# Performance work log

Hardware: AMD Instinct MI355X
Metric: run time of the kernel (lower is better)

## Reference

```python
import jax, jax.numpy as jnp
import numpy as np
import math

SR = 16000        # sample_rate
HOP = 512         # hop_length
FMIN = 20.0
N_BINS = 84
BPO = 12          # bins_per_octave
Q = 1.0 / (2.0 ** (1.0 / BPO) - 1.0)


def setup_inputs() -> dict:
    key = jax.random.key(0)
    waveform = jax.random.normal(key, (2560000,), dtype=jnp.float32)
    return {"waveform": waveform}


def _bin_kernel(wl: int, freq: float, dtype):
    """Windowed single-DFT-bin kernel matching torch.stft row `freq_bin`.
    Returns (2,1,wl) conv kernel: [real, imag] parts of conj(e^{-2pi i f n / wl}) * hann.
    """
    n = np.arange(wl)
    # torch.hann_window default is periodic: 0.5*(1 - cos(2*pi*n/N))
    w = 0.5 - 0.5 * np.cos(2.0 * np.pi * n / wl)
    fb = min(int(freq * wl / SR), wl // 2)  # onesided stft has wl//2+1 rows
    ang = 2.0 * np.pi * fb * n / wl
    kr = (w * np.cos(ang)).astype(np.float32)
    ki = (-w * np.sin(ang)).astype(np.float32)
    return jnp.asarray(np.stack([kr, ki])[:, None, :], dtype=dtype)


def reference(waveform) -> jnp.ndarray:
    L = waveform.shape[-1]
    num_frames = (L - HOP) // HOP + 1  # matches torch code's frame count
    rows = []
    for k in range(N_BINS):
        freq = FMIN * 2.0 ** (k / BPO)
        wl = min(int(SR * Q / freq), L // 4)
        if wl < 32:  # torch code skips these bins (row stays zero)
            rows.append(jnp.zeros((num_frames,), waveform.dtype))
            continue
        pad = wl // 2  # torch.stft center=True reflect padding
        xpad = jnp.pad(waveform, (pad, pad), mode="reflect")
        kern = _bin_kernel(wl, freq, waveform.dtype)
        # strided correlation == extracting one DFT bin of every stft frame
        out = jax.lax.conv_general_dilated(
            xpad[None, None, :], kern, window_strides=(HOP,), padding="VALID"
        )[0]  # (2, n_frames_k)
        mag = jnp.sqrt(out[0] ** 2 + out[1] ** 2)
        mf = min(mag.shape[0], num_frames)
        rows.append(jnp.zeros((num_frames,), waveform.dtype).at[:mf].set(mag[:mf]))
    return jnp.stack(rows)[None]  # (1, n_bins, num_frames)
```

## Files before the change

### kernel.cpp

```cpp
#include <hip/hip_runtime.h>
#include <math.h>

#define L_IN   2560000
#define HOP    512
#define NB     84
#define NF     5000
#define PAD0   6726
#define XPLEN  2573452
#define XBLEN2 2637824
#define NTIL   80
#define SLOTS  7
#define NBLK   (NTIL*SLOTS)
#define TSTEPS 251

#define XB_NB  1288
#define AG_NB  502

#define LDS_SZ 70656

#define XB_B 0
#define AG_B 5275648
#define P_B  7331840

typedef short bf16x8 __attribute__((ext_vector_type(8)));
typedef float f32x16 __attribute__((ext_vector_type(16)));

__device__ inline unsigned short f2bf(float f) {
  unsigned int u = __float_as_uint(f);
  return (unsigned short)((u + 0x7fffu + ((u >> 16) & 1u)) >> 16);
}

__device__ inline void load16(void* l, const void* g) {
  __builtin_amdgcn_global_load_lds((const __attribute__((address_space(1))) void*)g,
                                   (__attribute__((address_space(3))) void*)l, 16, 0, 0);
}

__global__ __launch_bounds__(256) void k_prep(const float* __restrict__ x,
                                              unsigned short* __restrict__ xb,
                                              unsigned short* __restrict__ Ag) {
  if (blockIdx.x < XB_NB) {
    int i8 = (blockIdx.x * 256 + threadIdx.x) * 8;
    bf16x8 o;
    int u0 = i8 - PAD0;
    if (u0 >= 0 && u0 + 8 <= L_IN) {
      const float2* p = (const float2*)(x + u0);
#pragma unroll
      for (int j = 0; j < 4; ++j) {
        float2 v = p[j];
        o[2 * j]     = (short)f2bf(v.x);
        o[2 * j + 1] = (short)f2bf(v.y);
      }
    } else {
#pragma unroll
      for (int j = 0; j < 8; ++j) {
        int i = i8 + j;
        float v = 0.f;
        if (i < XPLEN) {
          int u = i - PAD0;
          if (u < 0) u = -u;
          else if (u >= L_IN) u = 2 * L_IN - 2 - u;
          v = x[u];
        }
        o[j] = (short)f2bf(v);
      }
    }
    *(bf16x8*)(xb + i8) = o;
  } else {
    int g = (blockIdx.x - XB_NB) * 256 + threadIdx.x;
    int s = g >> 9, w = g & 511;
    int im = w >> 8, kk = (w >> 6) & 3, lane = w & 63;
    int mt  = (s < 211) ? 0 : ((s < 245) ? 1 : 2);
    int mst = (mt == 0) ? 0 : ((mt == 1) ? 211 : 245);
    int kst = (mt == 0) ? 0 : ((mt == 1) ? 5632 : 6528);
    int tap0 = kst + (s - mst) * 64 + kk * 16 + ((lane >> 5) << 3);
    int row = im * 32 + (lane & 31);
    int bin = mt * 32 + (row >> 1);
    bf16x8 vv;
    if (bin >= NB) {
#pragma unroll
      for (int j = 0; j < 8; ++j) vv[j] = 0;
    } else {
      double q    = 1.0 / (pow(2.0, 1.0 / 12.0) - 1.0);
      double freq = 20.0 * pow(2.0, (double)bin / 12.0);
      int wl = (int)(16000.0 * q / freq);
      if (wl > L_IN / 4) wl = L_IN / 4;
      int pad = wl >> 1;
      int fbq = (int)(freq * (double)wl / 16000.0);
      if (fbq > wl / 2) fbq = wl / 2;
      int isIm = row & 1;
      float invwl = 1.0f / (float)wl;
#pragma unroll
      for (int j = 0; j < 8; ++j) {
        int n = tap0 + j - (PAD0 - pad);
        float v = 0.f;
        if (n >= 0 && n < wl) {
          float wn = 0.5f - 0.5f * cosf(6.2831853071795865f * ((float)n * invwl));
          int m = (fbq * n) % wl;
          float a = 6.2831853071795865f * ((float)m * invwl);
          v = isIm ? (-wn * sinf(a)) : (wn * cosf(a));
        }
        vv[j] = (short)f2bf(v);
      }
    }
    *(bf16x8*)(Ag + ((size_t)s * 4096 + im * 2048 + kk * 512 + lane * 8)) = vv;
  }
}

struct AF { bf16x8 f[2][4]; };

__device__ inline void loadA(AF& a, const char* Ag, int s, int lane) {
  const char* p = Ag + ((size_t)s << 13) + lane * 16;
#pragma unroll
  for (int im = 0; im < 2; ++im)
#pragma unroll
    for (int kk = 0; kk < 4; ++kk)
      a.f[im][kk] = *(const bf16x8*)(p + im * 4096 + kk * 1024);
}

__device__ inline void stepC(const AF& a, int l, int lane, const char* Bw,
                             f32x16 acc[2][2]) {
  bf16x8 bf[2][4];
  int tb = l * 128 + ((lane >> 5) << 4);
#pragma unroll
  for (int in_ = 0; in_ < 2; ++in_) {
    int ob = (in_ * 32 + (lane & 31)) * 1024 + tb;
#pragma unroll
    for (int kk = 0; kk < 4; ++kk) {
      int o = ob + kk * 32;
      o ^= ((o >> 10) & 15) << 4;
      bf[in_][kk] = *(const bf16x8*)(Bw + o);
    }
  }
  __builtin_amdgcn_s_setprio(1);
#pragma unroll
  for (int kk = 0; kk < 4; ++kk)
#pragma unroll
    for (int im = 0; im < 2; ++im)
#pragma unroll
      for (int in_ = 0; in_ < 2; ++in_)
        acc[im][in_] = __builtin_amdgcn_mfma_f32_32x32x16_bf16(
            a.f[im][kk], bf[in_][kk], acc[im][in_], 0, 0, 0);
  __builtin_amdgcn_s_setprio(0);
}

__global__ __launch_bounds__(256, 2) void k_gemm(const unsigned short* __restrict__ Ag,
                                                 const unsigned short* __restrict__ xb,
                                                 float* __restrict__ P,
                                                 float* __restrict__ out) {
  extern __shared__ char lds[];
  const int tid = threadIdx.x, lane = tid & 63, wv = tid >> 6;

  int bid = blockIdx.x;
  int lid = (bid & 7) * (NBLK / 8) + (bid >> 3);
  int nt = lid / SLOTS, c = lid - nt * SLOTS;
  const int gs_[7] = {0, 43, 85, 127, 169, 211, 245};
  const int ns_[7] = {43, 42, 42, 42, 42, 34, 6};
  const int kb_[7] = {0, 2752, 5440, 8128, 10816, 5632, 6528};
  int gs = gs_[c], ns = ns_[c], kb = kb_[c];
  int nch = (64512 + 128 * ns + 1023) >> 10;

  const char* xsrc = (const char*)xb + (size_t)nt * 65536 + (size_t)kb * 2;
  for (int ci = wv; ci < nch; ci += 4)
    load16(lds + ci * 1024, xsrc + ci * 1024 + ((lane * 16) ^ ((ci & 15) << 4)));
  __builtin_amdgcn_sched_barrier(0);

  const char* Ab = (const char*)Ag;
  int nks = (ns - wv + 3) >> 2;
  AF a0, a1, a2;
  int s0 = gs + wv, s1 = gs + wv + 4, s2 = gs + wv + 8;
  loadA(a0, Ab, s0 > 250 ? 250 : s0, lane);
  loadA(a1, Ab, s1 > 250 ? 250 : s1, lane);
  loadA(a2, Ab, s2 > 250 ? 250 : s2, lane);

  f32x16 acc[2][2];
#pragma unroll
  for (int i = 0; i < 2; ++i)
#pragma unroll
    for (int j = 0; j < 2; ++j)
#pragma unroll
      for (int e = 0; e < 16; ++e) acc[i][j][e] = 0.f;

  asm volatile("s_waitcnt vmcnt(24)" ::: "memory");
  __syncthreads();

  int i = 0;
  while (i + 3 <= nks) {
    stepC(a0, wv + 4 * i, lane, lds, acc);
    if (i + 3 < nks) loadA(a0, Ab, gs + wv + 4 * (i + 3), lane);
    stepC(a1, wv + 4 * (i + 1), lane, lds, acc);
    if (i + 4 < nks) loadA(a1, Ab, gs + wv + 4 * (i + 4), lane);
    stepC(a2, wv + 4 * (i + 2), lane, lds, acc);
    if (i + 5 < nks) loadA(a2, Ab, gs + wv + 4 * (i + 5), lane);
    i += 3;
  }
  if (i < nks)     stepC(a0, wv + 4 * i, lane, lds, acc);
  if (i + 1 < nks) stepC(a1, wv + 4 * (i + 1), lane, lds, acc);
  if (i + 2 < nks) stepC(a2, wv + 4 * (i + 2), lane, lds, acc);

  __syncthreads();
  float* Cw = (float*)(lds + wv * 16384);
#pragma unroll
  for (int im = 0; im < 2; ++im)
#pragma unroll
    for (int in_ = 0; in_ < 2; ++in_) {
      f32x16 v = acc[im][in_];
      int col = in_ * 32 + (lane & 31);
      int rb  = im * 32 + ((lane >> 5) << 2);
#pragma unroll
      for (int r = 0; r < 16; ++r) {
        int row = rb + (r & 3) + 8 * (r >> 2);
        Cw[row * 64 + col] = v[r];
      }
    }
  __syncthreads();
  const float* L0 = (const float*)lds;
  if (c < 5) {
    float* Pb = P + ((size_t)(nt * 5 + c) << 12);
#pragma unroll
    for (int e = 0; e < 16; ++e) {
      int idx = e * 256 + tid;
      Pb[idx] = L0[idx] + L0[idx + 4096] + L0[idx + 8192] + L0[idx + 12288];
    }
  } else {
    int bb = (c == 5) ? 32 : 64;
#pragma unroll
    for (int e = 0; e < 8; ++e) {
      int p = e * 256 + tid;
      int bl = p >> 6, fl = p & 63;
      int r0 = (bl * 2) * 64 + fl, r1 = r0 + 64;
      float re = L0[r0] + L0[r0 + 4096] + L0[r0 + 8192] + L0[r0 + 12288];
      float iv = L0[r1] + L0[r1 + 4096] + L0[r1 + 8192] + L0[r1 + 12288];
      int b = bb + bl, col = nt * 64 + fl;
      if (b < NB && col < NF)
        out[(size_t)b * NF + col] = sqrtf(re * re + iv * iv);
    }
  }
}

__global__ __launch_bounds__(256) void k_mag(const float* __restrict__ P,
                                             float* __restrict__ out) {
  int col = blockIdx.x * 256 + threadIdx.x;
  int b = blockIdx.y;
  if (col >= NF) return;
  int nt = col >> 6, fl = col & 63;
  const float* Pt = P + ((size_t)(nt * 5) << 12);
  float re = 0.f, iv = 0.f;
#pragma unroll
  for (int c = 0; c < 5; ++c) {
    const float* Pb = Pt + ((size_t)c << 12);
    re += Pb[(2 * b) * 64 + fl];
    iv += Pb[(2 * b + 1) * 64 + fl];
  }
  out[(size_t)b * NF + col] = sqrtf(re * re + iv * iv);
}

extern "C" void kernel_launch(void* const* d_in, const int* in_sizes, int n_in,
                              void* d_out, int out_size, void* d_ws, size_t ws_size,
                              hipStream_t stream) {
  const float* x = (const float*)d_in[0];
  char* ws = (char*)d_ws;
  unsigned short* xb = (unsigned short*)(ws + XB_B);
  unsigned short* Ag = (unsigned short*)(ws + AG_B);
  float* P           = (float*)(ws + P_B);
  float* out = (float*)d_out;

  hipFuncSetAttribute((const void*)k_gemm,
                      hipFuncAttributeMaxDynamicSharedMemorySize, LDS_SZ);

  hipLaunchKernelGGL(k_prep, dim3(XB_NB + AG_NB), dim3(256), 0, stream, x, xb, Ag);
  hipLaunchKernelGGL(k_gemm, dim3(NBLK), dim3(256), LDS_SZ, stream, Ag, xb, P, out);
  hipLaunchKernelGGL(k_mag, dim3(20, 32), dim3(256), 0, stream, P, out);
}
```

Before: 33.14 us.

## Widen GEMM frame tile to 128 columns with 8-wave blocks

```diff
diff --git a/kernel.cpp b/kernel.cpp
--- a/kernel.cpp
+++ b/kernel.cpp
@@ -8,15 +8,13 @@
 #define PAD0   6726
 #define XPLEN  2573452
 #define XBLEN2 2637824
-#define NTIL   80
-#define SLOTS  7
+#define NTIL   40
+#define SLOTS  6
 #define NBLK   (NTIL*SLOTS)
-#define TSTEPS 251
-
 #define XB_NB  1288
 #define AG_NB  502
 
-#define LDS_SZ 70656
+#define LDS_SZ 137216
 
 #define XB_B 0
 #define AG_B 5275648
@@ -118,32 +116,29 @@
 }
 
 __device__ inline void stepC(const AF& a, int l, int lane, const char* Bw,
-                             f32x16 acc[2][2]) {
-  bf16x8 bf[2][4];
+                             f32x16 acc[2][4]) {
   int tb = l * 128 + ((lane >> 5) << 4);
 #pragma unroll
-  for (int in_ = 0; in_ < 2; ++in_) {
-    int ob = (in_ * 32 + (lane & 31)) * 1024 + tb;
+  for (int n = 0; n < 4; ++n) {
+    bf16x8 bf[4];
+    int ob = (n * 32 + (lane & 31)) * 1024 + tb;
 #pragma unroll
     for (int kk = 0; kk < 4; ++kk) {
       int o = ob + kk * 32;
       o ^= ((o >> 10) & 15) << 4;
-      bf[in_][kk] = *(const bf16x8*)(Bw + o);
-    }
-  }
-  __builtin_amdgcn_s_setprio(1);
-#pragma unroll
-  for (int kk = 0; kk < 4; ++kk)
-#pragma unroll
-    for (int im = 0; im < 2; ++im)
-#pragma unroll
-      for (int in_ = 0; in_ < 2; ++in_)
-        acc[im][in_] = __builtin_amdgcn_mfma_f32_32x32x16_bf16(
-            a.f[im][kk], bf[in_][kk], acc[im][in_], 0, 0, 0);
-  __builtin_amdgcn_s_setprio(0);
-}
-
-__global__ __launch_bounds__(256, 2) void k_gemm(const unsigned short* __restrict__ Ag,
+      bf[kk] = *(const bf16x8*)(Bw + o);
+    }
+    __builtin_amdgcn_s_setprio(1);
+#pragma unroll
+    for (int kk = 0; kk < 4; ++kk) {
+      acc[0][n] = __builtin_amdgcn_mfma_f32_32x32x16_bf16(a.f[0][kk], bf[kk], acc[0][n], 0, 0, 0);
+      acc[1][n] = __builtin_amdgcn_mfma_f32_32x32x16_bf16(a.f[1][kk], bf[kk], acc[1][n], 0, 0, 0);
+    }
+    __builtin_amdgcn_s_setprio(0);
+  }
+}
+
+__global__ __launch_bounds__(512, 2) void k_gemm(const unsigned short* __restrict__ Ag,
                                                  const unsigned short* __restrict__ xb,
                                                  float* __restrict__ P,
                                                  float* __restrict__ out) {
@@ -153,87 +148,87 @@
   int bid = blockIdx.x;
   int lid = (bid & 7) * (NBLK / 8) + (bid >> 3);
   int nt = lid / SLOTS, c = lid - nt * SLOTS;
-  const int gs_[7] = {0, 43, 85, 127, 169, 211, 245};
-  const int ns_[7] = {43, 42, 42, 42, 42, 34, 6};
-  const int kb_[7] = {0, 2752, 5440, 8128, 10816, 5632, 6528};
+  const int gs_[6] = {0, 53, 106, 159, 211, 245};
+  const int ns_[6] = {53, 53, 53, 52, 34, 6};
+  const int kb_[6] = {0, 3392, 6784, 10176, 5632, 6528};
   int gs = gs_[c], ns = ns_[c], kb = kb_[c];
-  int nch = (64512 + 128 * ns + 1023) >> 10;
-
-  const char* xsrc = (const char*)xb + (size_t)nt * 65536 + (size_t)kb * 2;
-  for (int ci = wv; ci < nch; ci += 4)
+  int nch = (130048 + 128 * ns + 1023) >> 10;
+
+  const char* xsrc = (const char*)xb + (size_t)nt * 131072 + (size_t)kb * 2;
+  for (int ci = wv; ci < nch; ci += 8)
     load16(lds + ci * 1024, xsrc + ci * 1024 + ((lane * 16) ^ ((ci & 15) << 4)));
   __builtin_amdgcn_sched_barrier(0);
 
   const char* Ab = (const char*)Ag;
-  int nks = (ns - wv + 3) >> 2;
-  AF a0, a1, a2;
-  int s0 = gs + wv, s1 = gs + wv + 4, s2 = gs + wv + 8;
+  int nks = (ns - wv + 7) >> 3;
+  AF a0, a1;
+  int s0 = gs + wv, s1 = gs + wv + 8;
   loadA(a0, Ab, s0 > 250 ? 250 : s0, lane);
   loadA(a1, Ab, s1 > 250 ? 250 : s1, lane);
-  loadA(a2, Ab, s2 > 250 ? 250 : s2, lane);
-
-  f32x16 acc[2][2];
+
+  f32x16 acc[2][4];
 #pragma unroll
   for (int i = 0; i < 2; ++i)
 #pragma unroll
-    for (int j = 0; j < 2; ++j)
+    for (int j = 0; j < 4; ++j)
 #pragma unroll
       for (int e = 0; e < 16; ++e) acc[i][j][e] = 0.f;
 
-  asm volatile("s_waitcnt vmcnt(24)" ::: "memory");
+  asm volatile("s_waitcnt vmcnt(16)" ::: "memory");
   __syncthreads();
 
   int i = 0;
-  while (i + 3 <= nks) {
-    stepC(a0, wv + 4 * i, lane, lds, acc);
-    if (i + 3 < nks) loadA(a0, Ab, gs + wv + 4 * (i + 3), lane);
-    stepC(a1, wv + 4 * (i + 1), lane, lds, acc);
-    if (i + 4 < nks) loadA(a1, Ab, gs + wv + 4 * (i + 4), lane);
-    stepC(a2, wv + 4 * (i + 2), lane, lds, acc);
-    if (i + 5 < nks) loadA(a2, Ab, gs + wv + 4 * (i + 5), lane);
-    i += 3;
-  }
-  if (i < nks)     stepC(a0, wv + 4 * i, lane, lds, acc);
-  if (i + 1 < nks) stepC(a1, wv + 4 * (i + 1), lane, lds, acc);
-  if (i + 2 < nks) stepC(a2, wv + 4 * (i + 2), lane, lds, acc);
+  for (; i + 2 <= nks; i += 2) {
+    stepC(a0, wv + 8 * i, lane, lds, acc);
+    int sa = gs + wv + 8 * (i + 2); if (sa > 250) sa = 250;
+    loadA(a0, Ab, sa, lane);
+    stepC(a1, wv + 8 * (i + 1), lane, lds, acc);
+    int sb = gs + wv + 8 * (i + 3); if (sb > 250) sb = 250;
+    loadA(a1, Ab, sb, lane);
+  }
+  if (i < nks) stepC(a0, wv + 8 * i, lane, lds, acc);
 
   __syncthreads();
-  float* Cw = (float*)(lds + wv * 16384);
-#pragma unroll
-  for (int im = 0; im < 2; ++im)
-#pragma unroll
-    for (int in_ = 0; in_ < 2; ++in_) {
-      f32x16 v = acc[im][in_];
-      int col = in_ * 32 + (lane & 31);
-      int rb  = im * 32 + ((lane >> 5) << 2);
-#pragma unroll
-      for (int r = 0; r < 16; ++r) {
-        int row = rb + (r & 3) + 8 * (r >> 2);
-        Cw[row * 64 + col] = v[r];
-      }
-    }
-  __syncthreads();
-  const float* L0 = (const float*)lds;
-  if (c < 5) {
-    float* Pb = P + ((size_t)(nt * 5 + c) << 12);
-#pragma unroll
-    for (int e = 0; e < 16; ++e) {
-      int idx = e * 256 + tid;
-      Pb[idx] = L0[idx] + L0[idx + 4096] + L0[idx + 8192] + L0[idx + 12288];
-    }
-  } else {
-    int bb = (c == 5) ? 32 : 64;
-#pragma unroll
-    for (int e = 0; e < 8; ++e) {
-      int p = e * 256 + tid;
-      int bl = p >> 6, fl = p & 63;
-      int r0 = (bl * 2) * 64 + fl, r1 = r0 + 64;
-      float re = L0[r0] + L0[r0 + 4096] + L0[r0 + 8192] + L0[r0 + 12288];
-      float iv = L0[r1] + L0[r1 + 4096] + L0[r1 + 8192] + L0[r1 + 12288];
-      int b = bb + bl, col = nt * 64 + fl;
-      if (b < NB && col < NF)
-        out[(size_t)b * NF + col] = sqrtf(re * re + iv * iv);
-    }
+  float* Pb = P + ((size_t)(nt * 4 + c) << 13);
+#pragma unroll
+  for (int h = 0; h < 2; ++h) {
+    float* Cw = (float*)(lds + wv * 16384);
+#pragma unroll
+    for (int im = 0; im < 2; ++im)
+#pragma unroll
+      for (int n2 = 0; n2 < 2; ++n2) {
+        f32x16 v = acc[im][2 * h + n2];
+        int col = n2 * 32 + (lane & 31);
+        int rb  = im * 32 + ((lane >> 5) << 2);
+#pragma unroll
+        for (int r = 0; r < 16; ++r) {
+          int row = rb + (r & 3) + 8 * (r >> 2);
+          Cw[row * 64 + col] = v[r];
+        }
+      }
+    __syncthreads();
+    const float* L0 = (const float*)lds;
+#pragma unroll
+    for (int e = 0; e < 4; ++e) {
+      int p = e * 512 + tid;
+      int rp = p >> 6, cl = p & 63;
+      float re = 0.f, iv = 0.f;
+#pragma unroll
+      for (int w = 0; w < 8; ++w) {
+        re += L0[w * 4096 + (2 * rp) * 64 + cl];
+        iv += L0[w * 4096 + (2 * rp + 1) * 64 + cl];
+      }
+      if (c < 4) {
+        Pb[(2 * rp) * 128 + h * 64 + cl]     = re;
+        Pb[(2 * rp + 1) * 128 + h * 64 + cl] = iv;
+      } else {
+        int b = ((c == 4) ? 32 : 64) + rp;
+        int colg = nt * 128 + h * 64 + cl;
+        if (b < NB && colg < NF)
+          out[(size_t)b * NF + colg] = sqrtf(re * re + iv * iv);
+      }
+    }
+    __syncthreads();
   }
 }
 
@@ -242,14 +237,14 @@
   int col = blockIdx.x * 256 + threadIdx.x;
   int b = blockIdx.y;
   if (col >= NF) return;
-  int nt = col >> 6, fl = col & 63;
-  const float* Pt = P + ((size_t)(nt * 5) << 12);
+  int nt = col >> 7, cl = col & 127;
+  const float* Pt = P + ((size_t)(nt * 4) << 13);
   float re = 0.f, iv = 0.f;
 #pragma unroll
-  for (int c = 0; c < 5; ++c) {
-    const float* Pb = Pt + ((size_t)c << 12);
-    re += Pb[(2 * b) * 64 + fl];
-    iv += Pb[(2 * b + 1) * 64 + fl];
+  for (int cc = 0; cc < 4; ++cc) {
+    const float* Pbc = Pt + ((size_t)cc << 13);
+    re += Pbc[(2 * b) * 128 + cl];
+    iv += Pbc[(2 * b + 1) * 128 + cl];
   }
   out[(size_t)b * NF + col] = sqrtf(re * re + iv * iv);
 }
@@ -268,6 +263,6 @@
                       hipFuncAttributeMaxDynamicSharedMemorySize, LDS_SZ);
 
   hipLaunchKernelGGL(k_prep, dim3(XB_NB + AG_NB), dim3(256), 0, stream, x, xb, Ag);
-  hipLaunchKernelGGL(k_gemm, dim3(NBLK), dim3(256), LDS_SZ, stream, Ag, xb, P, out);
+  hipLaunchKernelGGL(k_gemm, dim3(NBLK), dim3(512), LDS_SZ, stream, Ag, xb, P, out);
   hipLaunchKernelGGL(k_mag, dim3(20, 32), dim3(256), 0, stream, P, out);
 }
```

New measurement: 33.03 us. Within noise of the previous version (-0.3%).

## Software-pipeline LDS B-fragment reads against MFMAs and remap blocks to XCDs

Applied to the files above, without the earlier changes.

```diff
diff --git a/kernel.cpp b/kernel.cpp
--- a/kernel.cpp
+++ b/kernel.cpp
@@ -11,8 +11,6 @@
 #define NTIL   80
 #define SLOTS  7
 #define NBLK   (NTIL*SLOTS)
-#define TSTEPS 251
-
 #define XB_NB  1288
 #define AG_NB  502
 
@@ -117,29 +115,25 @@
       a.f[im][kk] = *(const bf16x8*)(p + im * 4096 + kk * 1024);
 }
 
-__device__ inline void stepC(const AF& a, int l, int lane, const char* Bw,
-                             f32x16 acc[2][2]) {
-  bf16x8 bf[2][4];
+__device__ inline void readB(bf16x8 bf[4], const char* Bw, int l, int g, int lane) {
   int tb = l * 128 + ((lane >> 5) << 4);
-#pragma unroll
-  for (int in_ = 0; in_ < 2; ++in_) {
-    int ob = (in_ * 32 + (lane & 31)) * 1024 + tb;
-#pragma unroll
-    for (int kk = 0; kk < 4; ++kk) {
-      int o = ob + kk * 32;
-      o ^= ((o >> 10) & 15) << 4;
-      bf[in_][kk] = *(const bf16x8*)(Bw + o);
-    }
-  }
+  int ob = (g * 32 + (lane & 31)) * 1024 + tb;
+#pragma unroll
+  for (int kk = 0; kk < 4; ++kk) {
+    int o = ob + kk * 32;
+    o ^= ((o >> 10) & 15) << 4;
+    bf[kk] = *(const bf16x8*)(Bw + o);
+  }
+}
+
+__device__ inline void mfma8(const AF& a, const bf16x8 bf[4],
+                             f32x16& accA, f32x16& accB) {
   __builtin_amdgcn_s_setprio(1);
 #pragma unroll
-  for (int kk = 0; kk < 4; ++kk)
-#pragma unroll
-    for (int im = 0; im < 2; ++im)
-#pragma unroll
-      for (int in_ = 0; in_ < 2; ++in_)
-        acc[im][in_] = __builtin_amdgcn_mfma_f32_32x32x16_bf16(
-            a.f[im][kk], bf[in_][kk], acc[im][in_], 0, 0, 0);
+  for (int kk = 0; kk < 4; ++kk) {
+    accA = __builtin_amdgcn_mfma_f32_32x32x16_bf16(a.f[0][kk], bf[kk], accA, 0, 0, 0);
+    accB = __builtin_amdgcn_mfma_f32_32x32x16_bf16(a.f[1][kk], bf[kk], accB, 0, 0, 0);
+  }
   __builtin_amdgcn_s_setprio(0);
 }
 
@@ -151,8 +145,9 @@
   const int tid = threadIdx.x, lane = tid & 63, wv = tid >> 6;
 
   int bid = blockIdx.x;
-  int lid = (bid & 7) * (NBLK / 8) + (bid >> 3);
-  int nt = lid / SLOTS, c = lid - nt * SLOTS;
+  int xcd = bid & 7, loc = bid >> 3;
+  int c = loc / 10, ntl = loc - c * 10;
+  int nt = xcd * 10 + ntl;
   const int gs_[7] = {0, 43, 85, 127, 169, 211, 245};
   const int ns_[7] = {43, 42, 42, 42, 42, 34, 6};
   const int kb_[7] = {0, 2752, 5440, 8128, 10816, 5632, 6528};
@@ -183,19 +178,61 @@
   asm volatile("s_waitcnt vmcnt(24)" ::: "memory");
   __syncthreads();
 
+  bf16x8 bA[4], bB[4];
+  readB(bA, lds, wv, 0, lane);
+
   int i = 0;
   while (i + 3 <= nks) {
-    stepC(a0, wv + 4 * i, lane, lds, acc);
-    if (i + 3 < nks) loadA(a0, Ab, gs + wv + 4 * (i + 3), lane);
-    stepC(a1, wv + 4 * (i + 1), lane, lds, acc);
-    if (i + 4 < nks) loadA(a1, Ab, gs + wv + 4 * (i + 4), lane);
-    stepC(a2, wv + 4 * (i + 2), lane, lds, acc);
-    if (i + 5 < nks) loadA(a2, Ab, gs + wv + 4 * (i + 5), lane);
+    {
+      int l = wv + 4 * i;
+      readB(bB, lds, l, 1, lane);
+      mfma8(a0, bA, acc[0][0], acc[1][0]);
+      int ln = (i + 1 < nks) ? (wv + 4 * (i + 1)) : l;
+      readB(bA, lds, ln, 0, lane);
+      mfma8(a0, bB, acc[0][1], acc[1][1]);
+      if (i + 3 < nks) loadA(a0, Ab, gs + wv + 4 * (i + 3), lane);
+    }
+    {
+      int l = wv + 4 * (i + 1);
+      readB(bB, lds, l, 1, lane);
+      mfma8(a1, bA, acc[0][0], acc[1][0]);
+      int ln = (i + 2 < nks) ? (wv + 4 * (i + 2)) : l;
+      readB(bA, lds, ln, 0, lane);
+      mfma8(a1, bB, acc[0][1], acc[1][1]);
+      if (i + 4 < nks) loadA(a1, Ab, gs + wv + 4 * (i + 4), lane);
+    }
+    {
+      int l = wv + 4 * (i + 2);
+      readB(bB, lds, l, 1, lane);
+      mfma8(a2, bA, acc[0][0], acc[1][0]);
+      int ln = (i + 3 < nks) ? (wv + 4 * (i + 3)) : l;
+      readB(bA, lds, ln, 0, lane);
+      mfma8(a2, bB, acc[0][1], acc[1][1]);
+      if (i + 5 < nks) loadA(a2, Ab, gs + wv + 4 * (i + 5), lane);
+    }
     i += 3;
   }
-  if (i < nks)     stepC(a0, wv + 4 * i, lane, lds, acc);
-  if (i + 1 < nks) stepC(a1, wv + 4 * (i + 1), lane, lds, acc);
-  if (i + 2 < nks) stepC(a2, wv + 4 * (i + 2), lane, lds, acc);
+  if (i < nks) {
+    int l = wv + 4 * i;
+    readB(bB, lds, l, 1, lane);
+    mfma8(a0, bA, acc[0][0], acc[1][0]);
+    int ln = (i + 1 < nks) ? (wv + 4 * (i + 1)) : l;
+    readB(bA, lds, ln, 0, lane);
+    mfma8(a0, bB, acc[0][1], acc[1][1]);
+    if (i + 1 < nks) {
+      int l1 = wv + 4 * (i + 1);
+      readB(bB, lds, l1, 1, lane);
+      mfma8(a1, bA, acc[0][0], acc[1][0]);
+      int l2 = (i + 2 < nks) ? (wv + 4 * (i + 2)) : l1;
+      readB(bA, lds, l2, 0, lane);
+      mfma8(a1, bB, acc[0][1], acc[1][1]);
+      if (i + 2 < nks) {
+        readB(bB, lds, wv + 4 * (i + 2), 1, lane);
+        mfma8(a2, bA, acc[0][0], acc[1][0]);
+        mfma8(a2, bB, acc[0][1], acc[1][1]);
+      }
+    }
+  }
 
   __syncthreads();
   float* Cw = (float*)(lds + wv * 16384);
```

New measurement: 32.58 us. About the same (-1.7%).
